# Kernel optimization log

Hardware: AMD Instinct MI355X
Metric: run time of the kernel (lower is better)

## Reference

```python
import jax, jax.numpy as jnp
import numpy as np

NUM_EXPERTS = 16
HIDDEN = 2048
INTER = HIDDEN * 2
TOP_K = 2
BATCH = 1024


def setup_inputs() -> dict:
    key = jax.random.key(0)
    ks = jax.random.split(key, 7)
    tokens = jax.random.normal(ks[0], (BATCH, HIDDEN), dtype=jnp.float32)
    topk_indices = jax.random.randint(ks[1], (BATCH, TOP_K), 0, NUM_EXPERTS, dtype=jnp.int64)
    topk_weights = jax.random.uniform(ks[2], (BATCH, TOP_K), dtype=jnp.float32)
    w1 = jax.random.normal(ks[3], (NUM_EXPERTS, HIDDEN, INTER), dtype=jnp.float32)
    b1 = jax.random.normal(ks[4], (NUM_EXPERTS, INTER), dtype=jnp.float32)
    w2 = jax.random.normal(ks[5], (NUM_EXPERTS, INTER, HIDDEN), dtype=jnp.float32)
    b2 = jax.random.normal(ks[6], (NUM_EXPERTS, HIDDEN), dtype=jnp.float32)
    return {"tokens": tokens, "topk_indices": topk_indices, "topk_weights": topk_weights,
            "w1": w1, "b1": b1, "w2": w2, "b2": b2}


def reference(tokens, topk_indices, topk_weights, w1, b1, w2, b2):
    # Mathematically identical to the torch per-token gather + bmm chain:
    #   out[t,k] = relu(tokens[t] @ w1[e] + b1[e]) @ w2[e] + b2[e],  e = topk_indices[t,k]
    # Computed densely over all experts (avoids materializing per-token weight
    # gathers of size [B*K, H, 2H]); gradients w.r.t. unselected experts are zero
    # since their outputs are discarded by the gather.
    h = jax.nn.relu(jnp.einsum('td,edi->tei', tokens, w1) + b1[None, :, :])   # [T,E,2H]
    out_all = jnp.einsum('tei,eio->teo', h, w2) + b2[None, :, :]              # [T,E,H]
    out_k = jnp.take_along_axis(out_all, topk_indices[:, :, None], axis=1)    # [T,K,H]
    return jnp.sum(out_k * topk_weights[:, :, None], axis=1)                  # [T,H]
```

## Files before the change

### kernel.cpp

```cpp
#include <hip/hip_runtime.h>
#include <stdint.h>

#define E_N 16
#define HID 2048
#define INTER_D 4096
#define NPAIR 2048
#define NTOK 1024
#define CAP 256

typedef __attribute__((ext_vector_type(8))) short bf16x8;
typedef __attribute__((ext_vector_type(4))) float f32x4;

static __device__ __forceinline__ unsigned short f2bf(float f) {
  union { float f; unsigned int u; } x; x.f = f;
  unsigned int r = x.u + 0x7fffu + ((x.u >> 16) & 1u);
  return (unsigned short)(r >> 16);
}

static __device__ __forceinline__ unsigned int cvt_pk_bf16(float lo, float hi) {
  unsigned int u;
  asm("v_cvt_pk_bf16_f32 %0, %1, %2" : "=v"(u) : "v"(lo), "v"(hi));
  return u;
}

__global__ void route_kernel(const int* __restrict__ idx, int* __restrict__ counts,
                             int* __restrict__ gidlist) {
  __shared__ int cnt[E_N];
  const int tid = threadIdx.x;
  if (tid < E_N) cnt[tid] = 0;
  for (int j = tid; j < E_N * CAP; j += 256) gidlist[j] = 0;
  __syncthreads();
  for (int p = tid; p < NPAIR; p += 256) {
    int e = idx[p] & 15;
    int pos = atomicAdd(&cnt[e], 1);
    if (pos < CAP) gidlist[e * CAP + pos] = p;
  }
  __syncthreads();
  if (tid < E_N) counts[tid] = (cnt[tid] < CAP) ? cnt[tid] : CAP;
}

__global__ void prep_a_kernel(const float* __restrict__ tok, unsigned short* __restrict__ A1) {
  const int i = (blockIdx.x * 256 + threadIdx.x) * 4;
  const float4 v = *reinterpret_cast<const float4*>(tok + i);
  uint2 o;
  o.x = cvt_pk_bf16(v.x, v.y);
  o.y = cvt_pk_bf16(v.z, v.w);
  *reinterpret_cast<uint2*>(A1 + i) = o;
}

template <int KDT, int NDIM, int MODE, int KSPLIT>
__global__ __launch_bounds__(512, 4) void moe_gemm_kernel(
    const unsigned short* __restrict__ Asrc,
    const float* __restrict__ W,
    const float* __restrict__ bias,
    const float* __restrict__ tw,
    const int* __restrict__ counts,
    const int* __restrict__ gidlist,
    unsigned short* __restrict__ Hout,
    float* __restrict__ Oout) {
  constexpr int KLOC = KDT / KSPLIT;
  constexpr int NK = KLOC / 64;
  constexpr int NB = NDIM / 128;
  constexpr int PG = NB * KSPLIT;
  const int bid = blockIdx.x;
  const int q = bid >> 3;
  const int e = (bid & 7) + 8 * (q / PG);
  const int j = q % PG;
  const int nc = j / KSPLIT;
  const int kh = j % KSPLIT;
  const int ne = counts[e];
  if (ne <= 0) return;
  const int n0 = nc * 128;
  const int tid = threadIdx.x;
  const int lane = tid & 63;
  const int wv = tid >> 6;
  const int wm = wv >> 2;
  const int wn = wv & 3;

  extern __shared__ char smem[];
  char* Ab0 = smem;
  char* Ab1 = smem + 32768;
  char* Bs  = smem + 65536;

  const int glist0 = e * CAP;

  const int c16 = (lane & 7) ^ ((lane >> 3) & 7);
  int aoff[4];
#pragma unroll
  for (int i = 0; i < 4; ++i) {
    const int row = wv * 32 + i * 8 + (lane >> 3);
    const int gid = gidlist[glist0 + row];
    const int arow = (MODE == 0) ? (gid >> 1) : gid;
    aoff[i] = arow * KDT + kh * KLOC + c16 * 8;
  }
  auto stageA = [&](int t, char* buf) {
#pragma unroll
    for (int i = 0; i < 4; ++i) {
      char* dst = buf + (wv * 4 + i) * 1024;
      __builtin_amdgcn_global_load_lds(
          (const __attribute__((address_space(1))) void*)(Asrc + aoff[i] + t * 64),
          (__attribute__((address_space(3))) void*)dst, 16, 0, 0);
    }
  };

  const int n4 = (tid & 31) * 4;
  const int k4 = (tid >> 5) * 4;
  const float* wbase = W + ((long)e * KDT + (long)kh * KLOC) * NDIM + n0 + n4;
  int bby[4];
#pragma unroll
  for (int c = 0; c < 4; ++c)
    bby[c] = (((n4 + c) * 128) + k4 * 2) ^ ((tid & 7) << 4);

  f32x4 b0, b1, b2, b3;
  auto loadB = [&](int t) {
    const float* p = wbase + (long)(t * 64 + k4) * NDIM;
    b0 = *reinterpret_cast<const f32x4*>(p);
    b1 = *reinterpret_cast<const f32x4*>(p + NDIM);
    b2 = *reinterpret_cast<const f32x4*>(p + 2 * NDIM);
    b3 = *reinterpret_cast<const f32x4*>(p + 3 * NDIM);
  };
  auto writeB = [&]() {
#pragma unroll
    for (int c = 0; c < 4; ++c) {
      unsigned long long u =
          (unsigned long long)cvt_pk_bf16(b0[c], b1[c]) |
          ((unsigned long long)cvt_pk_bf16(b2[c], b3[c]) << 32);
      *reinterpret_cast<unsigned long long*>(Bs + bby[c]) = u;
    }
  };

  const int rl = lane & 15;
  const int kg = lane >> 4;
  int abyte[2], bbF[2][2];
#pragma unroll
  for (int ks = 0; ks < 2; ++ks)
    abyte[ks] = (wm * 128 + rl) * 128 + (((ks * 4 + kg) ^ (rl & 7)) << 4);
#pragma unroll
  for (int nf = 0; nf < 2; ++nf) {
    const int n = wn * 32 + nf * 16 + rl;
#pragma unroll
    for (int ks = 0; ks < 2; ++ks)
      bbF[nf][ks] = ((n * 128) + (ks * 32 + kg * 8) * 2) ^ (((n >> 2) & 7) << 4);
  }

  f32x4 acc[8][2];
#pragma unroll
  for (int mf = 0; mf < 8; ++mf)
#pragma unroll
    for (int nf = 0; nf < 2; ++nf) acc[mf][nf] = (f32x4)(0.0f);

  const bool mact = (wm * 128) < ne;

  auto compute = [&](const char* Ab) {
#pragma unroll
    for (int ks = 0; ks < 2; ++ks) {
      bf16x8 bfr[2];
#pragma unroll
      for (int nf = 0; nf < 2; ++nf)
        bfr[nf] = *reinterpret_cast<const bf16x8*>(Bs + bbF[nf][ks]);
#pragma unroll
      for (int mf = 0; mf < 8; ++mf) {
        bf16x8 af = *reinterpret_cast<const bf16x8*>(Ab + abyte[ks] + mf * 2048);
        acc[mf][0] = __builtin_amdgcn_mfma_f32_16x16x32_bf16(af, bfr[0], acc[mf][0], 0, 0, 0);
        acc[mf][1] = __builtin_amdgcn_mfma_f32_16x16x32_bf16(af, bfr[1], acc[mf][1], 0, 0, 0);
      }
    }
  };

#define LGKM0 asm volatile("s_waitcnt lgkmcnt(0)" ::: "memory")
#define BARRIER asm volatile("s_barrier" ::: "memory")

  stageA(0, Ab0);
  stageA(1, Ab1);
  loadB(0);
  asm volatile("s_waitcnt vmcnt(0)" ::: "memory");
  writeB();
  loadB(1);
  LGKM0; BARRIER;

  for (int t = 0; t < NK - 2; ++t) {
    char* Ab = (t & 1) ? Ab1 : Ab0;
    if (mact) compute(Ab);
    LGKM0; BARRIER;
    stageA(t + 2, Ab);
    asm volatile("s_waitcnt vmcnt(4)" ::: "memory");
    writeB();
    loadB(t + 2);
    LGKM0; BARRIER;
  }

  if (mact) compute(Ab0);
  LGKM0; BARRIER;
  asm volatile("s_waitcnt vmcnt(0)" ::: "memory");
  writeB();
  LGKM0; BARRIER;
  if (mact) compute(Ab1);
#undef LGKM0
#undef BARRIER

  if (mact) {
    const int rg = (lane >> 4) * 4;
    float bc[2];
#pragma unroll
    for (int nf = 0; nf < 2; ++nf)
      bc[nf] = (MODE == 1 && kh != 0) ? 0.0f
             : bias[(long)e * NDIM + n0 + wn * 32 + nf * 16 + rl];
#pragma unroll
    for (int mf = 0; mf < 8; ++mf) {
#pragma unroll
      for (int r = 0; r < 4; ++r) {
        const int row = wm * 128 + mf * 16 + rg + r;
        if (row < ne) {
          const int gid = gidlist[glist0 + row];
#pragma unroll
          for (int nf = 0; nf < 2; ++nf) {
            const int col = n0 + wn * 32 + nf * 16 + rl;
            float v = acc[mf][nf][r] + bc[nf];
            if constexpr (MODE == 0) {
              v = fmaxf(v, 0.0f);
              Hout[(long)gid * NDIM + col] = f2bf(v);
            } else {
              v *= tw[gid];
              atomicAdd(Oout + (long)(gid >> 1) * NDIM + col, v);
            }
          }
        }
      }
    }
  }
}

extern "C" void kernel_launch(void* const* d_in, const int* in_sizes, int n_in,
                              void* d_out, int out_size, void* d_ws, size_t ws_size,
                              hipStream_t stream) {
  const float* tokens = (const float*)d_in[0];
  const int* idx      = (const int*)d_in[1];
  const float* tw     = (const float*)d_in[2];
  const float* w1     = (const float*)d_in[3];
  const float* b1     = (const float*)d_in[4];
  const float* w2     = (const float*)d_in[5];
  const float* b2     = (const float*)d_in[6];
  float* out = (float*)d_out;

  char* ws = (char*)d_ws;
  int* counts  = (int*)ws;
  int* gidlist = (int*)(ws + 1024);
  unsigned short* A1   = (unsigned short*)(ws + 32768);
  unsigned short* hbuf = (unsigned short*)(ws + 32768 + (size_t)NTOK * HID * 2);

  hipMemsetAsync(out, 0, (size_t)NTOK * HID * sizeof(float), stream);
  route_kernel<<<1, 256, 0, stream>>>(idx, counts, gidlist);
  prep_a_kernel<<<(NTOK * HID / 4) / 256, 256, 0, stream>>>(tokens, A1);

  hipFuncSetAttribute((const void*)moe_gemm_kernel<HID, INTER_D, 0, 1>,
                      hipFuncAttributeMaxDynamicSharedMemorySize, 81920);
  hipFuncSetAttribute((const void*)moe_gemm_kernel<INTER_D, HID, 1, 2>,
                      hipFuncAttributeMaxDynamicSharedMemorySize, 81920);

  moe_gemm_kernel<HID, INTER_D, 0, 1><<<512, 512, 81920, stream>>>(
      A1, w1, b1, nullptr, counts, gidlist, hbuf, nullptr);
  moe_gemm_kernel<INTER_D, HID, 1, 2><<<512, 512, 81920, stream>>>(
      hbuf, w2, b2, tw, counts, gidlist, nullptr, out);
}
```

Baseline: 241.7 us.

## Widen MoE GEMM N tile to 256 and cache gather ids in LDS

```diff
diff --git a/kernel.cpp b/kernel.cpp
--- a/kernel.cpp
+++ b/kernel.cpp
@@ -49,7 +49,7 @@
 }
 
 template <int KDT, int NDIM, int MODE, int KSPLIT>
-__global__ __launch_bounds__(512, 4) void moe_gemm_kernel(
+__global__ __launch_bounds__(512, 2) void moe_gemm_kernel(
     const unsigned short* __restrict__ Asrc,
     const float* __restrict__ W,
     const float* __restrict__ bias,
@@ -60,8 +60,8 @@
     float* __restrict__ Oout) {
   constexpr int KLOC = KDT / KSPLIT;
   constexpr int NK = KLOC / 64;
-  constexpr int NB = NDIM / 128;
-  constexpr int PG = NB * KSPLIT;
+  constexpr int NC = NDIM / 256;
+  constexpr int PG = NC * KSPLIT;
   const int bid = blockIdx.x;
   const int q = bid >> 3;
   const int e = (bid & 7) + 8 * (q / PG);
@@ -70,7 +70,7 @@
   const int kh = j % KSPLIT;
   const int ne = counts[e];
   if (ne <= 0) return;
-  const int n0 = nc * 128;
+  const int n0 = nc * 256;
   const int tid = threadIdx.x;
   const int lane = tid & 63;
   const int wv = tid >> 6;
@@ -81,88 +81,106 @@
   char* Ab0 = smem;
   char* Ab1 = smem + 32768;
   char* Bs  = smem + 65536;
-
-  const int glist0 = e * CAP;
-
+  __shared__ int sgid[CAP];
+  if (tid < CAP) sgid[tid] = gidlist[e * CAP + tid];
+  __syncthreads();
+
+  const bool astage = (wv * 32) < ne;
   const int c16 = (lane & 7) ^ ((lane >> 3) & 7);
-  int aoff[4];
+  const unsigned short* arp[4];
 #pragma unroll
   for (int i = 0; i < 4; ++i) {
     const int row = wv * 32 + i * 8 + (lane >> 3);
-    const int gid = gidlist[glist0 + row];
-    const int arow = (MODE == 0) ? (gid >> 1) : gid;
-    aoff[i] = arow * KDT + kh * KLOC + c16 * 8;
+    const int gid = sgid[row];
+    const long arow = (MODE == 0) ? (gid >> 1) : gid;
+    arp[i] = Asrc + arow * (long)KDT + kh * KLOC + c16 * 8;
   }
   auto stageA = [&](int t, char* buf) {
+    if (!astage) return;
 #pragma unroll
     for (int i = 0; i < 4; ++i) {
       char* dst = buf + (wv * 4 + i) * 1024;
       __builtin_amdgcn_global_load_lds(
-          (const __attribute__((address_space(1))) void*)(Asrc + aoff[i] + t * 64),
+          (const __attribute__((address_space(1))) void*)(arp[i] + t * 64),
           (__attribute__((address_space(3))) void*)dst, 16, 0, 0);
     }
   };
 
-  const int n4 = (tid & 31) * 4;
-  const int k4 = (tid >> 5) * 4;
-  const float* wbase = W + ((long)e * KDT + (long)kh * KLOC) * NDIM + n0 + n4;
-  int bby[4];
-#pragma unroll
-  for (int c = 0; c < 4; ++c)
-    bby[c] = (((n4 + c) * 128) + k4 * 2) ^ ((tid & 7) << 4);
-
-  f32x4 b0, b1, b2, b3;
+  const int nq = (tid & 31) * 4;
+  const int kq = (tid >> 5) * 4;
+  const float* wb0 = W + ((long)e * KDT + (long)kh * KLOC) * NDIM + n0 + nq;
+  const float* wb1 = wb0 + 128;
+  int bby0[4], bby1[4];
+#pragma unroll
+  for (int c = 0; c < 4; ++c) {
+    const int key = (((nq + c) >> 2) & 7) << 4;
+    bby0[c] = (((nq + c) * 128) + kq * 2) ^ key;
+    bby1[c] = bby0[c] + 16384;
+  }
+
+  f32x4 b00, b01, b02, b03, b10, b11, b12, b13;
   auto loadB = [&](int t) {
-    const float* p = wbase + (long)(t * 64 + k4) * NDIM;
-    b0 = *reinterpret_cast<const f32x4*>(p);
-    b1 = *reinterpret_cast<const f32x4*>(p + NDIM);
-    b2 = *reinterpret_cast<const f32x4*>(p + 2 * NDIM);
-    b3 = *reinterpret_cast<const f32x4*>(p + 3 * NDIM);
+    const float* p0 = wb0 + (long)(t * 64 + kq) * NDIM;
+    const float* p1 = wb1 + (long)(t * 64 + kq) * NDIM;
+    b00 = *reinterpret_cast<const f32x4*>(p0);
+    b01 = *reinterpret_cast<const f32x4*>(p0 + NDIM);
+    b02 = *reinterpret_cast<const f32x4*>(p0 + 2 * NDIM);
+    b03 = *reinterpret_cast<const f32x4*>(p0 + 3 * NDIM);
+    b10 = *reinterpret_cast<const f32x4*>(p1);
+    b11 = *reinterpret_cast<const f32x4*>(p1 + NDIM);
+    b12 = *reinterpret_cast<const f32x4*>(p1 + 2 * NDIM);
+    b13 = *reinterpret_cast<const f32x4*>(p1 + 3 * NDIM);
   };
   auto writeB = [&]() {
 #pragma unroll
     for (int c = 0; c < 4; ++c) {
-      unsigned long long u =
-          (unsigned long long)cvt_pk_bf16(b0[c], b1[c]) |
-          ((unsigned long long)cvt_pk_bf16(b2[c], b3[c]) << 32);
-      *reinterpret_cast<unsigned long long*>(Bs + bby[c]) = u;
+      unsigned long long u0 =
+          (unsigned long long)cvt_pk_bf16(b00[c], b01[c]) |
+          ((unsigned long long)cvt_pk_bf16(b02[c], b03[c]) << 32);
+      *reinterpret_cast<unsigned long long*>(Bs + bby0[c]) = u0;
+      unsigned long long u1 =
+          (unsigned long long)cvt_pk_bf16(b10[c], b11[c]) |
+          ((unsigned long long)cvt_pk_bf16(b12[c], b13[c]) << 32);
+      *reinterpret_cast<unsigned long long*>(Bs + bby1[c]) = u1;
     }
   };
 
   const int rl = lane & 15;
   const int kg = lane >> 4;
-  int abyte[2], bbF[2][2];
+  int abyte[2], bbF[4][2];
 #pragma unroll
   for (int ks = 0; ks < 2; ++ks)
     abyte[ks] = (wm * 128 + rl) * 128 + (((ks * 4 + kg) ^ (rl & 7)) << 4);
 #pragma unroll
-  for (int nf = 0; nf < 2; ++nf) {
-    const int n = wn * 32 + nf * 16 + rl;
+  for (int nf = 0; nf < 4; ++nf) {
+    const int nl = (wn & 1) * 64 + nf * 16 + rl;
 #pragma unroll
     for (int ks = 0; ks < 2; ++ks)
-      bbF[nf][ks] = ((n * 128) + (ks * 32 + kg * 8) * 2) ^ (((n >> 2) & 7) << 4);
-  }
-
-  f32x4 acc[8][2];
+      bbF[nf][ks] = (wn >> 1) * 16384 +
+                    (((nl * 128) + (ks * 32 + kg * 8) * 2) ^ (((nl >> 2) & 7) << 4));
+  }
+
+  f32x4 acc[8][4];
 #pragma unroll
   for (int mf = 0; mf < 8; ++mf)
 #pragma unroll
-    for (int nf = 0; nf < 2; ++nf) acc[mf][nf] = (f32x4)(0.0f);
+    for (int nf = 0; nf < 4; ++nf) acc[mf][nf] = (f32x4)(0.0f);
 
   const bool mact = (wm * 128) < ne;
 
   auto compute = [&](const char* Ab) {
 #pragma unroll
     for (int ks = 0; ks < 2; ++ks) {
-      bf16x8 bfr[2];
-#pragma unroll
-      for (int nf = 0; nf < 2; ++nf)
+      bf16x8 bfr[4];
+#pragma unroll
+      for (int nf = 0; nf < 4; ++nf)
         bfr[nf] = *reinterpret_cast<const bf16x8*>(Bs + bbF[nf][ks]);
 #pragma unroll
       for (int mf = 0; mf < 8; ++mf) {
         bf16x8 af = *reinterpret_cast<const bf16x8*>(Ab + abyte[ks] + mf * 2048);
-        acc[mf][0] = __builtin_amdgcn_mfma_f32_16x16x32_bf16(af, bfr[0], acc[mf][0], 0, 0, 0);
-        acc[mf][1] = __builtin_amdgcn_mfma_f32_16x16x32_bf16(af, bfr[1], acc[mf][1], 0, 0, 0);
+#pragma unroll
+        for (int nf = 0; nf < 4; ++nf)
+          acc[mf][nf] = __builtin_amdgcn_mfma_f32_16x16x32_bf16(af, bfr[nf], acc[mf][nf], 0, 0, 0);
       }
     }
   };
@@ -200,21 +218,21 @@
 
   if (mact) {
     const int rg = (lane >> 4) * 4;
-    float bc[2];
-#pragma unroll
-    for (int nf = 0; nf < 2; ++nf)
+    float bc[4];
+#pragma unroll
+    for (int nf = 0; nf < 4; ++nf)
       bc[nf] = (MODE == 1 && kh != 0) ? 0.0f
-             : bias[(long)e * NDIM + n0 + wn * 32 + nf * 16 + rl];
+             : bias[(long)e * NDIM + n0 + wn * 64 + nf * 16 + rl];
 #pragma unroll
     for (int mf = 0; mf < 8; ++mf) {
 #pragma unroll
       for (int r = 0; r < 4; ++r) {
         const int row = wm * 128 + mf * 16 + rg + r;
         if (row < ne) {
-          const int gid = gidlist[glist0 + row];
-#pragma unroll
-          for (int nf = 0; nf < 2; ++nf) {
-            const int col = n0 + wn * 32 + nf * 16 + rl;
+          const int gid = sgid[row];
+#pragma unroll
+          for (int nf = 0; nf < 4; ++nf) {
+            const int col = n0 + wn * 64 + nf * 16 + rl;
             float v = acc[mf][nf][r] + bc[nf];
             if constexpr (MODE == 0) {
               v = fmaxf(v, 0.0f);
@@ -253,12 +271,12 @@
   prep_a_kernel<<<(NTOK * HID / 4) / 256, 256, 0, stream>>>(tokens, A1);
 
   hipFuncSetAttribute((const void*)moe_gemm_kernel<HID, INTER_D, 0, 1>,
-                      hipFuncAttributeMaxDynamicSharedMemorySize, 81920);
+                      hipFuncAttributeMaxDynamicSharedMemorySize, 98304);
   hipFuncSetAttribute((const void*)moe_gemm_kernel<INTER_D, HID, 1, 2>,
-                      hipFuncAttributeMaxDynamicSharedMemorySize, 81920);
-
-  moe_gemm_kernel<HID, INTER_D, 0, 1><<<512, 512, 81920, stream>>>(
+                      hipFuncAttributeMaxDynamicSharedMemorySize, 98304);
+
+  moe_gemm_kernel<HID, INTER_D, 0, 1><<<256, 512, 98304, stream>>>(
       A1, w1, b1, nullptr, counts, gidlist, hbuf, nullptr);
-  moe_gemm_kernel<INTER_D, HID, 1, 2><<<512, 512, 81920, stream>>>(
+  moe_gemm_kernel<INTER_D, HID, 1, 2><<<256, 512, 98304, stream>>>(
       hbuf, w2, b2, tw, counts, gidlist, nullptr, out);
 }
```

Result: faster. 236.2 us (-2.3%).
